# Optimization experiments

Hardware: AMD Instinct MI355X
Metric: run time of the kernel (lower is better)

The kernel has to match this reference:

```python
import jax, jax.numpy as jnp
import numpy as np

D = 1024
SPARSITY = 0.1  # fraction of non-zero weights per layer (DeepR)


def _make_theta_sign(key, d1, d2, density):
    # DeepR weight_sampler_strict_number: theta > 0 exactly on the active
    # (non-zero) connections, theta <= 0 (dormant) elsewhere; sign is +-1.
    k1, k2, k3 = jax.random.split(key, 3)
    mask = jax.random.uniform(k1, (d1, d2)) < density
    mag = jnp.abs(jax.random.normal(k2, (d1, d2))) / np.sqrt(d1)
    th = jnp.where(mask, mag, -mag)
    sign = jnp.where(jax.random.uniform(k3, (d1, d2)) < 0.5, -1.0, 1.0).astype(jnp.float32)
    return th.astype(jnp.float32), sign


def setup_inputs() -> dict:
    key = jax.random.key(0)
    kx, k1, k2 = jax.random.split(key, 3)
    x = jax.random.normal(kx, (8, 4096, D), dtype=jnp.float32)
    th1, sign1 = _make_theta_sign(k1, D, D, SPARSITY)
    th2, sign2 = _make_theta_sign(k2, D, D, SPARSITY)
    return {"x": x, "th1": th1, "sign1": sign1, "th2": th2, "sign2": sign2, "relu": 1}


def reference(x, th1, sign1, th2, sign2, relu):
    # Layer i: reconstruct sparse weight w = theta * sign * (theta > 0),
    # then dense matmul (+ optional relu). dropout=0, binarize=False.
    for th, sign in ((th1, sign1), (th2, sign2)):
        w = th * sign * (th > 0)
        x = jnp.matmul(x, w)              # [B, S, D]
        if relu:
            x = jax.nn.relu(x)
    return x
```

## Files before the change

kernel.cpp:

```cpp
#include <hip/hip_runtime.h>
#include <stdint.h>

#define DD 1024
#define MROWS 32768
#define NTK 32

typedef __attribute__((ext_vector_type(8))) short short8;
typedef __attribute__((ext_vector_type(8))) unsigned short ushort8;
typedef __attribute__((ext_vector_type(4))) float f32x4;

static __device__ __forceinline__ unsigned short f2bf(float f) {
    union { float f; uint32_t u; } c;
    c.f = f;
    uint32_t u = c.u;
    u += 0x7FFFu + ((u >> 16) & 1u);
    return (unsigned short)(u >> 16);
}

static __device__ __forceinline__ void gload_lds16(const void* g, void* l) {
    __builtin_amdgcn_global_load_lds(
        (const __attribute__((address_space(1))) uint32_t*)g,
        (__attribute__((address_space(3))) uint32_t*)l,
        16, 0, 0);
}

#define SBAR() __builtin_amdgcn_s_barrier()
#define SCHED_FENCE() __builtin_amdgcn_sched_barrier(0)

__global__ __launch_bounds__(256) void build_wT_kernel(
        const float* __restrict__ th1, const float* __restrict__ sg1,
        const float* __restrict__ th2, const float* __restrict__ sg2,
        unsigned short* __restrict__ wT1, unsigned short* __restrict__ wT2) {
    __shared__ unsigned short tile[64][65];
    const float* th = blockIdx.z ? th2 : th1;
    const float* sg = blockIdx.z ? sg2 : sg1;
    unsigned short* wT = blockIdx.z ? wT2 : wT1;
    const int bk = blockIdx.x, bn = blockIdx.y, t = threadIdx.x;
    #pragma unroll
    for (int i = 0; i < 4; ++i) {
        int idx = i * 256 + t;
        int r = idx >> 4, cg = idx & 15;
        size_t base = (size_t)(bk * 64 + r) * DD + bn * 64 + cg * 4;
        const float4 tv = *(const float4*)&th[base];
        const float4 sv = *(const float4*)&sg[base];
        tile[r][cg * 4 + 0] = f2bf(tv.x > 0.f ? tv.x * sv.x : 0.f);
        tile[r][cg * 4 + 1] = f2bf(tv.y > 0.f ? tv.y * sv.y : 0.f);
        tile[r][cg * 4 + 2] = f2bf(tv.z > 0.f ? tv.z * sv.z : 0.f);
        tile[r][cg * 4 + 3] = f2bf(tv.w > 0.f ? tv.w * sv.w : 0.f);
    }
    __syncthreads();
    #pragma unroll
    for (int i = 0; i < 4; ++i) {
        int idx = i * 256 + t;
        int nr = idx >> 4, kg = idx & 15;
        uint32_t lo = tile[kg * 4 + 0][nr] | ((uint32_t)tile[kg * 4 + 1][nr] << 16);
        uint32_t hi = tile[kg * 4 + 2][nr] | ((uint32_t)tile[kg * 4 + 3][nr] << 16);
        *(uint2*)&wT[(size_t)(bn * 64 + nr) * DD + bk * 64 + kg * 4] = make_uint2(lo, hi);
    }
}

template<bool A_FP32>
__global__ __launch_bounds__(256, A_FP32 ? 3 : 4) void gemm_db(
        const void* __restrict__ Ap,
        const unsigned short* __restrict__ Bt,
        void* __restrict__ Cp) {
    __shared__ unsigned short sB[2][128 * 32];
    __shared__ float          sAf[A_FP32 ? 2 * 128 * 32 : 2];
    __shared__ unsigned short sAh[A_FP32 ? 2 : 2 * 128 * 32];

    const int tid  = threadIdx.x;
    const int lane = tid & 63;
    const int wid  = tid >> 6;
    const int wm = wid >> 1, wn = wid & 1;
    const int fr = lane & 15, fq = lane >> 4;

    const int s = blockIdx.x;
    const int L = ((s & 7) << 8) + (s >> 3);
    const int bm = L >> 3;
    const int bn = L & 7;

    const unsigned short* bsrc =
        Bt + (size_t)(bn * 128 + wid * 32 + (lane >> 2)) * DD
           + ((lane & 3) ^ ((lane >> 2) & 3)) * 8;
    const unsigned short* ahsrc = nullptr;
    const float* afsrc = nullptr;
    if constexpr (A_FP32) {
        afsrc = (const float*)Ap + (size_t)(bm * 128 + wid * 32 + (lane >> 3)) * DD
                                 + ((lane & 7) ^ ((lane >> 3) & 7)) * 4;
    } else {
        ahsrc = (const unsigned short*)Ap + (size_t)(bm * 128 + wid * 32 + (lane >> 2)) * DD
                                          + ((lane & 3) ^ ((lane >> 2) & 3)) * 8;
    }

    auto stage = [&](int p, int kt) {
        #pragma unroll
        for (int j = 0; j < 2; ++j)
            gload_lds16(bsrc + (size_t)j * 16 * DD + kt * 32,
                        &sB[p][(wid * 32 + j * 16) * 32]);
        if constexpr (A_FP32) {
            #pragma unroll
            for (int j = 0; j < 4; ++j)
                gload_lds16(afsrc + (size_t)j * 8 * DD + kt * 32,
                            &sAf[(size_t)p * 128 * 32 + (wid * 32 + j * 8) * 32]);
        } else {
            #pragma unroll
            for (int j = 0; j < 2; ++j)
                gload_lds16(ahsrc + (size_t)j * 16 * DD + kt * 32,
                            &sAh[(size_t)p * 128 * 32 + (wid * 32 + j * 16) * 32]);
        }
    };

    const f32x4 vz = {0.f, 0.f, 0.f, 0.f};
    f32x4 acc[4][4];
    #pragma unroll
    for (int i = 0; i < 4; ++i)
        #pragma unroll
        for (int j = 0; j < 4; ++j) acc[i][j] = vz;

    stage(0, 0);

    #pragma unroll 1
    for (int t = 0; t < NTK; ++t) {
        const int p = t & 1;
        if (t + 1 < NTK) {
            stage(p ^ 1, t + 1);
            if constexpr (A_FP32) asm volatile("s_waitcnt vmcnt(6)" ::: "memory");
            else                  asm volatile("s_waitcnt vmcnt(4)" ::: "memory");
        } else {
            asm volatile("s_waitcnt vmcnt(0)" ::: "memory");
        }
        SBAR();
        SCHED_FENCE();

        short8 av[4], bv[4];
        #pragma unroll
        for (int ni = 0; ni < 4; ++ni) {
            int row = wn * 64 + ni * 16 + fr;
            bv[ni] = *(const short8*)((const char*)&sB[p][0]
                        + row * 64 + ((fq ^ (row & 3)) << 4));
        }
        if constexpr (A_FP32) {
            #pragma unroll
            for (int mi = 0; mi < 4; ++mi) {
                int row = wm * 64 + mi * 16 + fr;
                const char* base = (const char*)&sAf[(size_t)p * 128 * 32] + row * 128;
                f32x4 lo = *(const f32x4*)(base + ((((fq << 1) | 0) ^ (row & 7)) << 4));
                f32x4 hi = *(const f32x4*)(base + ((((fq << 1) | 1) ^ (row & 7)) << 4));
                short8 w;
                #pragma unroll
                for (int i = 0; i < 4; ++i) { w[i] = (short)f2bf(lo[i]); w[4 + i] = (short)f2bf(hi[i]); }
                av[mi] = w;
            }
        } else {
            #pragma unroll
            for (int mi = 0; mi < 4; ++mi) {
                int row = wm * 64 + mi * 16 + fr;
                av[mi] = *(const short8*)((const char*)&sAh[(size_t)p * 128 * 32]
                            + row * 64 + ((fq ^ (row & 3)) << 4));
            }
        }
        #pragma unroll
        for (int mi = 0; mi < 4; ++mi)
            #pragma unroll
            for (int ni = 0; ni < 4; ++ni)
                acc[mi][ni] = __builtin_amdgcn_mfma_f32_16x16x32_bf16(
                    av[mi], bv[ni], acc[mi][ni], 0, 0, 0);
        SBAR();
    }

    const int orow0 = bm * 128 + wm * 64 + fq * 4;
    const int ocol0 = bn * 128 + wn * 64 + fr;
    #pragma unroll
    for (int mi = 0; mi < 4; ++mi)
        #pragma unroll
        for (int ni = 0; ni < 4; ++ni)
            #pragma unroll
            for (int r = 0; r < 4; ++r) {
                float v = fmaxf(acc[mi][ni][r], 0.f);
                size_t off = (size_t)(orow0 + mi * 16 + r) * DD + (ocol0 + ni * 16);
                if (A_FP32) ((unsigned short*)Cp)[off] = f2bf(v);
                else        ((float*)Cp)[off] = v;
            }
}

__global__ __launch_bounds__(256) void fallback_fused(
        const float* __restrict__ x,
        const float* __restrict__ th1, const float* __restrict__ sg1,
        const float* __restrict__ th2, const float* __restrict__ sg2,
        float* __restrict__ out) {
    __shared__ float xr[8][DD];
    __shared__ float y1[8][DD];
    const int rb = blockIdx.x * 8;
    const int t = threadIdx.x;
    for (int r = 0; r < 8; ++r)
        for (int i = t; i < DD; i += 256)
            xr[r][i] = x[(size_t)(rb + r) * DD + i];
    __syncthreads();
    for (int jo = 0; jo < 4; ++jo) {
        const int j = jo * 256 + t;
        float a[8] = {0, 0, 0, 0, 0, 0, 0, 0};
        for (int k = 0; k < DD; ++k) {
            float tv = th1[(size_t)k * DD + j];
            float w = tv > 0.f ? tv * sg1[(size_t)k * DD + j] : 0.f;
            #pragma unroll
            for (int r = 0; r < 8; ++r) a[r] += xr[r][k] * w;
        }
        #pragma unroll
        for (int r = 0; r < 8; ++r) y1[r][j] = fmaxf(a[r], 0.f);
    }
    __syncthreads();
    for (int jo = 0; jo < 4; ++jo) {
        const int j = jo * 256 + t;
        float a[8] = {0, 0, 0, 0, 0, 0, 0, 0};
        for (int k = 0; k < DD; ++k) {
            float tv = th2[(size_t)k * DD + j];
            float w = tv > 0.f ? tv * sg2[(size_t)k * DD + j] : 0.f;
            #pragma unroll
            for (int r = 0; r < 8; ++r) a[r] += y1[r][k] * w;
        }
        #pragma unroll
        for (int r = 0; r < 8; ++r) out[(size_t)(rb + r) * DD + j] = fmaxf(a[r], 0.f);
    }
}

extern "C" void kernel_launch(void* const* d_in, const int* in_sizes, int n_in,
                              void* d_out, int out_size, void* d_ws, size_t ws_size,
                              hipStream_t stream) {
    const float* x   = (const float*)d_in[0];
    const float* th1 = (const float*)d_in[1];
    const float* sg1 = (const float*)d_in[2];
    const float* th2 = (const float*)d_in[3];
    const float* sg2 = (const float*)d_in[4];
    float* out = (float*)d_out;

    const size_t need = ((size_t)2 * 1024 * 1024 + (size_t)MROWS * 1024) * 2;
    if (ws_size >= need) {
        unsigned short* wT1 = (unsigned short*)d_ws;
        unsigned short* wT2 = wT1 + 1024 * 1024;
        unsigned short* Y1  = wT2 + 1024 * 1024;
        build_wT_kernel<<<dim3(16, 16, 2), 256, 0, stream>>>(th1, sg1, th2, sg2, wT1, wT2);
        gemm_db<true ><<<dim3((MROWS / 128) * 8), 256, 0, stream>>>(x,  wT1, Y1);
        gemm_db<false><<<dim3((MROWS / 128) * 8), 256, 0, stream>>>(Y1, wT2, out);
    } else {
        fallback_fused<<<MROWS / 8, 256, 0, stream>>>(x, th1, sg1, th2, sg2, out);
    }
}
```

Before: 240.6 us.

## Load A fragments directly to registers, deepen K tile to 64

The A operand is now read straight from global memory into MFMA register fragments instead of being staged through LDS. When A is fp32, it is converted with packed v_cvt_pk_bf16_f32 instructions. Only B is double-buffered in LDS, now with a K tile of 64 and an 8-way XOR swizzle, which halves the loop trip count. MFMA issue is wrapped in s_setprio, and the vmcnt waits are retuned to account for the outstanding A register loads. This removes A's LDS traffic and barrier pressure, at the cost of more VGPRs, less coalesced A loads (each lane reads 32 bytes per row), and hand-tuned wait counts that must match the exact load ordering.

```diff
diff --git a/kernel.cpp b/kernel.cpp
--- a/kernel.cpp
+++ b/kernel.cpp
@@ -3,7 +3,7 @@
 
 #define DD 1024
 #define MROWS 32768
-#define NTK 32
+#define NTK 16
 
 typedef __attribute__((ext_vector_type(8))) short short8;
 typedef __attribute__((ext_vector_type(8))) unsigned short ushort8;
@@ -25,7 +25,16 @@
 }
 
 #define SBAR() __builtin_amdgcn_s_barrier()
-#define SCHED_FENCE() __builtin_amdgcn_sched_barrier(0)
+#define SFENCE() __builtin_amdgcn_sched_barrier(0)
+
+static __device__ __forceinline__ short8 cvt8pk(f32x4 lo, f32x4 hi) {
+    union { short8 s; uint32_t u[4]; } r;
+    asm("v_cvt_pk_bf16_f32 %0, %1, %2" : "=v"(r.u[0]) : "v"(lo[0]), "v"(lo[1]));
+    asm("v_cvt_pk_bf16_f32 %0, %1, %2" : "=v"(r.u[1]) : "v"(lo[2]), "v"(lo[3]));
+    asm("v_cvt_pk_bf16_f32 %0, %1, %2" : "=v"(r.u[2]) : "v"(hi[0]), "v"(hi[1]));
+    asm("v_cvt_pk_bf16_f32 %0, %1, %2" : "=v"(r.u[3]) : "v"(hi[2]), "v"(hi[3]));
+    return r.s;
+}
 
 __global__ __launch_bounds__(256) void build_wT_kernel(
         const float* __restrict__ th1, const float* __restrict__ sg1,
@@ -60,17 +69,14 @@
 }
 
 template<bool A_FP32>
-__global__ __launch_bounds__(256, A_FP32 ? 3 : 4) void gemm_db(
+__global__ __launch_bounds__(256, 3) void gemm_ag(
         const void* __restrict__ Ap,
         const unsigned short* __restrict__ Bt,
         void* __restrict__ Cp) {
-    __shared__ unsigned short sB[2][128 * 32];
-    __shared__ float          sAf[A_FP32 ? 2 * 128 * 32 : 2];
-    __shared__ unsigned short sAh[A_FP32 ? 2 : 2 * 128 * 32];
-
-    const int tid  = threadIdx.x;
-    const int lane = tid & 63;
-    const int wid  = tid >> 6;
+    __shared__ unsigned short sB[2][128 * 64];
+
+    const int tid = threadIdx.x;
+    const int lane = tid & 63, wid = tid >> 6;
     const int wm = wid >> 1, wn = wid & 1;
     const int fr = lane & 15, fq = lane >> 4;
 
@@ -80,35 +86,19 @@
     const int bn = L & 7;
 
     const unsigned short* bsrc =
-        Bt + (size_t)(bn * 128 + wid * 32 + (lane >> 2)) * DD
-           + ((lane & 3) ^ ((lane >> 2) & 3)) * 8;
-    const unsigned short* ahsrc = nullptr;
-    const float* afsrc = nullptr;
-    if constexpr (A_FP32) {
-        afsrc = (const float*)Ap + (size_t)(bm * 128 + wid * 32 + (lane >> 3)) * DD
-                                 + ((lane & 7) ^ ((lane >> 3) & 7)) * 4;
-    } else {
-        ahsrc = (const unsigned short*)Ap + (size_t)(bm * 128 + wid * 32 + (lane >> 2)) * DD
-                                          + ((lane & 3) ^ ((lane >> 2) & 3)) * 8;
-    }
-
-    auto stage = [&](int p, int kt) {
-        #pragma unroll
-        for (int j = 0; j < 2; ++j)
-            gload_lds16(bsrc + (size_t)j * 16 * DD + kt * 32,
-                        &sB[p][(wid * 32 + j * 16) * 32]);
-        if constexpr (A_FP32) {
-            #pragma unroll
-            for (int j = 0; j < 4; ++j)
-                gload_lds16(afsrc + (size_t)j * 8 * DD + kt * 32,
-                            &sAf[(size_t)p * 128 * 32 + (wid * 32 + j * 8) * 32]);
-        } else {
-            #pragma unroll
-            for (int j = 0; j < 2; ++j)
-                gload_lds16(ahsrc + (size_t)j * 16 * DD + kt * 32,
-                            &sAh[(size_t)p * 128 * 32 + (wid * 32 + j * 16) * 32]);
-        }
+        Bt + (size_t)(bn * 128 + wid * 32 + (lane >> 3)) * DD
+           + ((lane & 7) ^ ((lane >> 3) & 7)) * 8;
+    auto stageB = [&](int p, int kt) {
+        #pragma unroll
+        for (int j = 0; j < 4; ++j)
+            gload_lds16(bsrc + (size_t)j * 8 * DD + kt * 64,
+                        &sB[p][(wid * 32 + j * 8) * 64]);
     };
+
+    const unsigned short* aB = nullptr;
+    const float* aF = nullptr;
+    if constexpr (A_FP32) aF = (const float*)Ap + (size_t)(bm * 128 + wm * 64 + fr) * DD;
+    else                  aB = (const unsigned short*)Ap + (size_t)(bm * 128 + wm * 64 + fr) * DD;
 
     const f32x4 vz = {0.f, 0.f, 0.f, 0.f};
     f32x4 acc[4][4];
@@ -117,54 +107,58 @@
         #pragma unroll
         for (int j = 0; j < 4; ++j) acc[i][j] = vz;
 
-    stage(0, 0);
+    stageB(0, 0);
 
     #pragma unroll 1
     for (int t = 0; t < NTK; ++t) {
         const int p = t & 1;
+
+        short8 av[4][2];
+        #pragma unroll
+        for (int mi = 0; mi < 4; ++mi)
+            #pragma unroll
+            for (int kk = 0; kk < 2; ++kk) {
+                if constexpr (A_FP32) {
+                    const float* pA = aF + (size_t)mi * 16 * DD + t * 64 + kk * 32 + fq * 8;
+                    f32x4 lo = *(const f32x4*)pA;
+                    f32x4 hi = *(const f32x4*)(pA + 4);
+                    av[mi][kk] = cvt8pk(lo, hi);
+                } else {
+                    av[mi][kk] = *(const short8*)(aB + (size_t)mi * 16 * DD + t * 64 + kk * 32 + fq * 8);
+                }
+            }
+
         if (t + 1 < NTK) {
-            stage(p ^ 1, t + 1);
-            if constexpr (A_FP32) asm volatile("s_waitcnt vmcnt(6)" ::: "memory");
-            else                  asm volatile("s_waitcnt vmcnt(4)" ::: "memory");
+            stageB(p ^ 1, t + 1);
+            if constexpr (A_FP32) asm volatile("s_waitcnt vmcnt(20)" ::: "memory");
+            else                  asm volatile("s_waitcnt vmcnt(12)" ::: "memory");
         } else {
-            asm volatile("s_waitcnt vmcnt(0)" ::: "memory");
+            if constexpr (A_FP32) asm volatile("s_waitcnt vmcnt(16)" ::: "memory");
+            else                  asm volatile("s_waitcnt vmcnt(8)" ::: "memory");
         }
         SBAR();
-        SCHED_FENCE();
-
-        short8 av[4], bv[4];
-        #pragma unroll
-        for (int ni = 0; ni < 4; ++ni) {
-            int row = wn * 64 + ni * 16 + fr;
-            bv[ni] = *(const short8*)((const char*)&sB[p][0]
-                        + row * 64 + ((fq ^ (row & 3)) << 4));
-        }
-        if constexpr (A_FP32) {
-            #pragma unroll
-            for (int mi = 0; mi < 4; ++mi) {
-                int row = wm * 64 + mi * 16 + fr;
-                const char* base = (const char*)&sAf[(size_t)p * 128 * 32] + row * 128;
-                f32x4 lo = *(const f32x4*)(base + ((((fq << 1) | 0) ^ (row & 7)) << 4));
-                f32x4 hi = *(const f32x4*)(base + ((((fq << 1) | 1) ^ (row & 7)) << 4));
-                short8 w;
+        SFENCE();
+
+        short8 bv[4][2];
+        #pragma unroll
+        for (int ni = 0; ni < 4; ++ni)
+            #pragma unroll
+            for (int kk = 0; kk < 2; ++kk) {
+                int row = wn * 64 + ni * 16 + fr;
+                bv[ni][kk] = *(const short8*)((const char*)&sB[p][0]
+                               + row * 128 + (((kk * 4 + fq) ^ (row & 7)) << 4));
+            }
+        __builtin_amdgcn_s_setprio(1);
+        #pragma unroll
+        for (int mi = 0; mi < 4; ++mi)
+            #pragma unroll
+            for (int ni = 0; ni < 4; ++ni)
                 #pragma unroll
-                for (int i = 0; i < 4; ++i) { w[i] = (short)f2bf(lo[i]); w[4 + i] = (short)f2bf(hi[i]); }
-                av[mi] = w;
-            }
-        } else {
-            #pragma unroll
-            for (int mi = 0; mi < 4; ++mi) {
-                int row = wm * 64 + mi * 16 + fr;
-                av[mi] = *(const short8*)((const char*)&sAh[(size_t)p * 128 * 32]
-                            + row * 64 + ((fq ^ (row & 3)) << 4));
-            }
-        }
-        #pragma unroll
-        for (int mi = 0; mi < 4; ++mi)
-            #pragma unroll
-            for (int ni = 0; ni < 4; ++ni)
-                acc[mi][ni] = __builtin_amdgcn_mfma_f32_16x16x32_bf16(
-                    av[mi], bv[ni], acc[mi][ni], 0, 0, 0);
+                for (int kk = 0; kk < 2; ++kk)
+                    acc[mi][ni] = __builtin_amdgcn_mfma_f32_16x16x32_bf16(
+                        av[mi][kk], bv[ni][kk], acc[mi][ni], 0, 0, 0);
+        __builtin_amdgcn_s_setprio(0);
+        SFENCE();
         SBAR();
     }
 
@@ -239,8 +233,8 @@
         unsigned short* wT2 = wT1 + 1024 * 1024;
         unsigned short* Y1  = wT2 + 1024 * 1024;
         build_wT_kernel<<<dim3(16, 16, 2), 256, 0, stream>>>(th1, sg1, th2, sg2, wT1, wT2);
-        gemm_db<true ><<<dim3((MROWS / 128) * 8), 256, 0, stream>>>(x,  wT1, Y1);
-        gemm_db<false><<<dim3((MROWS / 128) * 8), 256, 0, stream>>>(Y1, wT2, out);
+        gemm_ag<true ><<<dim3((MROWS / 128) * 8), 256, 0, stream>>>(x,  wT1, Y1);
+        gemm_ag<false><<<dim3((MROWS / 128) * 8), 256, 0, stream>>>(Y1, wT2, out);
     } else {
         fallback_fused<<<MROWS / 8, 256, 0, stream>>>(x, th1, sg1, th2, sg2, out);
     }
```

Result: slower. 438.5 us (+82.2%).
